# Optimization experiments

Measured on AMD Instinct MI355X. Metric: run time of the kernel, lower is better.

## Reference

```python
import jax, jax.numpy as jnp
import numpy as np

D_MODEL = 1024
N_HEADS = 16
D_HEAD = D_MODEL // N_HEADS
B, T = 2, 2048


def setup_inputs() -> dict:
    key = jax.random.key(0)
    ks = jax.random.split(key, 8)
    s = 1.0 / np.sqrt(D_MODEL)
    return {
        "x": jax.random.normal(ks[0], (B, T, D_MODEL), dtype=jnp.float32),
        "ln_g": jnp.ones((D_MODEL,), jnp.float32),
        "ln_b": jnp.zeros((D_MODEL,), jnp.float32),
        "w_qkv": jax.random.normal(ks[1], (D_MODEL, 3 * D_MODEL), jnp.float32) * s,
        "b_qkv": jnp.zeros((3 * D_MODEL,), jnp.float32),
        "w_gate": jax.random.normal(ks[2], (D_MODEL, D_MODEL), jnp.float32) * s,
        "b_gate": jnp.zeros((D_MODEL,), jnp.float32),
        "w_proj": jax.random.normal(ks[3], (D_MODEL, D_MODEL), jnp.float32) * s,
        "b_proj": jnp.zeros((D_MODEL,), jnp.float32),
    }


def reference(x, ln_g, ln_b, w_qkv, b_qkv, w_gate, b_gate, w_proj, b_proj):
    Bb, Tt, Dd = x.shape
    H, dh = N_HEADS, D_HEAD

    # LayerNorm (eps=1e-5, torch default)
    mu = jnp.mean(x, axis=-1, keepdims=True)
    var = jnp.mean((x - mu) ** 2, axis=-1, keepdims=True)
    x_norm = (x - mu) / jnp.sqrt(var + 1e-5) * ln_g + ln_b

    qkv = x_norm @ w_qkv + b_qkv
    q, k, v = jnp.split(qkv, 3, axis=-1)

    # concept gate on the RAW input x (not x_norm), normalized by its mean
    gate_sig = jax.nn.sigmoid(x @ w_gate + b_gate)
    gate_norm = gate_sig / (jnp.mean(gate_sig, axis=-1, keepdims=True) + 1e-5)
    q = q * gate_norm
    k = k * gate_norm

    # [B,T,D] -> [B,H,T,dh]
    def to_heads(t):
        return t.reshape(Bb, Tt, H, dh).transpose(0, 2, 1, 3)

    q, k, v = to_heads(q), to_heads(k), to_heads(v)

    q = jax.nn.elu(q) + 1.0
    k = jax.nn.elu(k) + 1.0

    # materialized outer-product cumsum (faithful to source formulation)
    kv = jnp.einsum("bhtd,bhtm->bhtdm", k, v)          # [B,H,T,dh,dh]
    kv_cumsum = jnp.cumsum(kv, axis=2)
    out_num = jnp.einsum("bhtd,bhtdm->bhtm", q, kv_cumsum)
    k_cumsum = jnp.cumsum(k, axis=2)
    out_den = jnp.einsum("bhtd,bhtd->bht", q, k_cumsum)[..., None] + 1e-5
    out = out_num / out_den                              # [B,H,T,dh]

    out = out.transpose(0, 2, 1, 3).reshape(Bb, Tt, Dd)
    return out @ w_proj + b_proj
```

## Files before the change

kernel.cpp:

```cpp
#include <hip/hip_runtime.h>
#include <math.h>

constexpr int D      = 1024;
constexpr int H      = 16;
constexpr int DH     = 64;
constexpr int Bb     = 2;
constexpr int T      = 2048;
constexpr int BT     = Bb * T;
constexpr int CHUNK  = 64;
constexpr int NC     = T / CHUNK;
constexpr int LS     = 72;

typedef __attribute__((ext_vector_type(8))) short bf16x8;
typedef __attribute__((ext_vector_type(4))) float f32x4;

#define GLOAD_LDS16(gp, lp) \
    __builtin_amdgcn_global_load_lds((const __attribute__((address_space(1))) void*)(gp), \
                                     (__attribute__((address_space(3))) void*)(lp), 16, 0, 0)

__device__ __forceinline__ short to_bf16(float f) {
    unsigned u = __float_as_uint(f);
    unsigned r = (u + 0x7fffu + ((u >> 16) & 1u)) >> 16;
    return (short)r;
}
__device__ __forceinline__ float bf2f(short s) {
    return __uint_as_float(((unsigned)(unsigned short)s) << 16);
}

__device__ __forceinline__ float block_sum_256(float v, float* sbuf) {
    #pragma unroll
    for (int off = 32; off > 0; off >>= 1) v += __shfl_down(v, off, 64);
    int lane = threadIdx.x & 63;
    int wid  = threadIdx.x >> 6;
    if (lane == 0) sbuf[wid] = v;
    __syncthreads();
    float r = (threadIdx.x < 4) ? sbuf[threadIdx.x] : 0.0f;
    r += __shfl_down(r, 2, 64);
    r += __shfl_down(r, 1, 64);
    if (threadIdx.x == 0) sbuf[0] = r;
    __syncthreads();
    float outv = sbuf[0];
    __syncthreads();
    return outv;
}

__device__ __forceinline__ float elu1(float x) {
    return x > 0.0f ? x + 1.0f : __expf(x);
}

__global__ __launch_bounds__(256) void pre_kernel(const float* __restrict__ x,
                                                  const float* __restrict__ g,
                                                  const float* __restrict__ b,
                                                  const float* __restrict__ wq,
                                                  const float* __restrict__ wg,
                                                  const float* __restrict__ wp,
                                                  short* __restrict__ ynb,
                                                  short* __restrict__ xbb,
                                                  short* __restrict__ wTcomb,
                                                  short* __restrict__ wTp,
                                                  float* __restrict__ gmean) {
    __shared__ float sbuf[4];
    __shared__ short tile[32][33];
    int bid = blockIdx.x;
    if (bid < BT) {
        int row = bid;
        if (threadIdx.x == 0) gmean[row] = 0.0f;
        const float* xr = x + (size_t)row * D;
        int c = threadIdx.x * 4;
        float4 xv = *(const float4*)(xr + c);
        float mu = block_sum_256(xv.x + xv.y + xv.z + xv.w, sbuf) * (1.0f / D);
        float d0 = xv.x - mu, d1 = xv.y - mu, d2 = xv.z - mu, d3 = xv.w - mu;
        float var = block_sum_256(d0*d0 + d1*d1 + d2*d2 + d3*d3, sbuf) * (1.0f / D);
        float rstd = rsqrtf(var + 1e-5f);
        float4 gv = *(const float4*)(g + c);
        float4 bv = *(const float4*)(b + c);
        short4 o, xo;
        o.x = to_bf16(d0 * rstd * gv.x + bv.x);
        o.y = to_bf16(d1 * rstd * gv.y + bv.y);
        o.z = to_bf16(d2 * rstd * gv.z + bv.z);
        o.w = to_bf16(d3 * rstd * gv.w + bv.w);
        xo.x = to_bf16(xv.x); xo.y = to_bf16(xv.y);
        xo.z = to_bf16(xv.z); xo.w = to_bf16(xv.w);
        *(short4*)(ynb + (size_t)row * D + c) = o;
        *(short4*)(xbb + (size_t)row * D + c) = xo;
    } else {
        int t2 = bid - BT;
        const float* W; short* Wt; int N; int t;
        if (t2 < 3072)      { W = wq; Wt = wTcomb;                       N = 3072; t = t2; }
        else if (t2 < 4096) { W = wg; Wt = wTcomb + (size_t)3072 * 1024; N = 1024; t = t2 - 3072; }
        else                { W = wp; Wt = wTp;                          N = 1024; t = t2 - 4096; }
        int ntiles = N >> 5;
        int nb = (t % ntiles) * 32, kb = (t / ntiles) * 32;
        int tx = threadIdx.x & 31, ty = threadIdx.x >> 5;
        #pragma unroll
        for (int i = 0; i < 4; ++i) {
            int k = kb + ty + i * 8;
            tile[ty + i * 8][tx] = to_bf16(W[(size_t)k * N + nb + tx]);
        }
        __syncthreads();
        #pragma unroll
        for (int i = 0; i < 4; ++i) {
            int n = nb + ty + i * 8;
            Wt[(size_t)n * 1024 + kb + tx] = tile[tx][ty + i * 8];
        }
    }
}

__global__ __launch_bounds__(256) void gemm_fused_qkvgate(const short* __restrict__ xnb,
                                                          const short* __restrict__ xb,
                                                          const short* __restrict__ Wt,
                                                          const float* __restrict__ b_qkv,
                                                          const float* __restrict__ b_gate,
                                                          short* __restrict__ qkvb,
                                                          short* __restrict__ sigb,
                                                          float* __restrict__ gmean) {
    constexpr int BK = 32, K = 1024;
    __shared__ short Als[128 * BK];
    __shared__ short Bls[128 * BK];

    const int bid   = blockIdx.x;
    const int xcd   = bid & 7;
    const int local = bid >> 3;
    const int cx = xcd & 3, ry = xcd >> 2;
    const int lx = local & 7, ly = local >> 3;
    const int bxx = cx * 8 + lx;
    const int byy = ry * 16 + ly;

    const int tid  = threadIdx.x;
    const int wave = tid >> 6;
    const int lane = tid & 63;
    const int row0 = byy * 128;
    const int col0 = bxx * 128;
    const bool isg = (col0 >= 3 * D);
    const short* A = isg ? xb : xnb;
    const int wm = (wave & 1) * 64;
    const int wn = (wave >> 1) * 64;

    f32x4 acc[4][4] = {};
    const int srow = lane >> 2;
    const int skk  = (lane & 3) * 8;
    const int fr = lane & 15;
    const int fk = (lane >> 4) * 8;

    for (int k0 = 0; k0 < K; k0 += BK) {
        __syncthreads();
        #pragma unroll
        for (int u = 0; u < 2; ++u) {
            int cchunk = wave * 2 + u;
            int r = cchunk * 16 + srow;
            GLOAD_LDS16(A  + (size_t)(row0 + r) * K + k0 + skk, &Als[cchunk * 512]);
            GLOAD_LDS16(Wt + (size_t)(col0 + r) * K + k0 + skk, &Bls[cchunk * 512]);
        }
        __syncthreads();

        bf16x8 af[4], bfr[4];
        #pragma unroll
        for (int i = 0; i < 4; ++i) {
            af[i]  = *(const bf16x8*)&Als[(wm + i * 16 + fr) * BK + fk];
            bfr[i] = *(const bf16x8*)&Bls[(wn + i * 16 + fr) * BK + fk];
        }
        #pragma unroll
        for (int mi = 0; mi < 4; ++mi)
            #pragma unroll
            for (int ni = 0; ni < 4; ++ni)
                acc[mi][ni] = __builtin_amdgcn_mfma_f32_16x16x32_bf16(af[mi], bfr[ni], acc[mi][ni], 0, 0, 0);
    }

    const int ccol  = lane & 15;
    const int crow4 = (lane >> 4) * 4;
    if (!isg) {
        #pragma unroll
        for (int mi = 0; mi < 4; ++mi) {
            #pragma unroll
            for (int ni = 0; ni < 4; ++ni) {
                int col = col0 + wn + ni * 16 + ccol;
                float bv = b_qkv[col];
                #pragma unroll
                for (int r = 0; r < 4; ++r) {
                    int row = row0 + wm + mi * 16 + crow4 + r;
                    qkvb[(size_t)row * (3 * D) + col] = to_bf16(acc[mi][ni][r] + bv);
                }
            }
        }
    } else {
        #pragma unroll
        for (int mi = 0; mi < 4; ++mi) {
            #pragma unroll
            for (int r = 0; r < 4; ++r) {
                int lrow = wm + mi * 16 + crow4 + r;
                float psum = 0.0f;
                #pragma unroll
                for (int ni = 0; ni < 4; ++ni) {
                    int col = col0 + wn + ni * 16 + ccol - 3 * D;
                    float v = acc[mi][ni][r] + b_gate[col];
                    float sv = 1.0f / (1.0f + __expf(-v));
                    sigb[(size_t)(row0 + lrow) * D + col] = to_bf16(sv);
                    psum += sv;
                }
                psum += __shfl_xor(psum, 1, 64);
                psum += __shfl_xor(psum, 2, 64);
                psum += __shfl_xor(psum, 4, 64);
                psum += __shfl_xor(psum, 8, 64);
                if (ccol == 0) atomicAdd(&gmean[row0 + lrow], psum);
            }
        }
    }
}

__global__ __launch_bounds__(256) void chunk_state_mfma(const short* __restrict__ qkvb,
                                                        const short* __restrict__ sigb,
                                                        const float* __restrict__ gmean,
                                                        float* __restrict__ Sc,
                                                        float* __restrict__ zc) {
    __shared__ short Kt[DH * LS];
    __shared__ short Vt[DH * LS];
    int idx = blockIdx.x;
    int c = idx & (NC - 1), h = (idx >> 5) & (H - 1), b = idx >> 9;
    size_t bt0 = (size_t)b * T + c * CHUNK;
    const short* kbase = qkvb + bt0 * (3 * D) + D + h * DH;
    const short* vbase = kbase + D;
    const short* sbase = sigb + bt0 * D + h * DH;
    int tid = threadIdx.x;

    #pragma unroll
    for (int l = 0; l < 2; ++l) {
        int i  = tid + l * 256;
        int t  = i >> 3;
        int d8 = (i & 7) * 8;
        float invm = 1.0f / (gmean[bt0 + t] * (1.0f / D) + 1e-5f);
        bf16x8 kv = *(const bf16x8*)(kbase + (size_t)t * (3 * D) + d8);
        bf16x8 vv = *(const bf16x8*)(vbase + (size_t)t * (3 * D) + d8);
        bf16x8 sg = *(const bf16x8*)(sbase + (size_t)t * D + d8);
        #pragma unroll
        for (int j = 0; j < 8; ++j) {
            float gn = bf2f(sg[j]) * invm;
            Kt[(d8 + j) * LS + t] = to_bf16(elu1(bf2f(kv[j]) * gn));
            Vt[(d8 + j) * LS + t] = vv[j];
        }
    }
    __syncthreads();

    const int wv = tid >> 6, lane = tid & 63;
    const int fr = lane & 15, quad = lane >> 4;
    const int fk = quad * 8, crow4 = quad * 4, ccol = lane & 15;
    const int mbase = wv * 16;

    bf16x8 af[2];
    af[0] = *(const bf16x8*)&Vt[(mbase + fr) * LS + fk];
    af[1] = *(const bf16x8*)&Vt[(mbase + fr) * LS + 32 + fk];

    f32x4 acc[4] = {};
    #pragma unroll
    for (int n = 0; n < 4; ++n) {
        #pragma unroll
        for (int ck = 0; ck < 2; ++ck) {
            bf16x8 bk = *(const bf16x8*)&Kt[(n * 16 + fr) * LS + ck * 32 + fk];
            acc[n] = __builtin_amdgcn_mfma_f32_16x16x32_bf16(af[ck], bk, acc[n], 0, 0, 0);
        }
    }

    float* Sd = Sc + (size_t)idx * (DH * DH);
    #pragma unroll
    for (int n = 0; n < 4; ++n)
        #pragma unroll
        for (int r = 0; r < 4; ++r)
            Sd[(mbase + crow4 + r) * DH + n * 16 + ccol] = acc[n][r];

    if (tid < DH) {
        float zs = 0.0f;
        for (int t = 0; t < CHUNK; ++t) zs += bf2f(Kt[tid * LS + t]);
        zc[(size_t)idx * DH + tid] = zs;
    }
}

__global__ __launch_bounds__(256) void chunk_prefix_kernel(const float* __restrict__ S,
                                                           short* __restrict__ Spb,
                                                           float* __restrict__ z) {
    int bh   = blockIdx.x >> 4;
    int part = blockIdx.x & 15;
    int e    = part * 256 + threadIdx.x;
    const float* Sb = S + (size_t)bh * NC * DH * DH;
    short* Pb = Spb + (size_t)bh * NC * DH * DH;
    float acc = 0.0f;
    for (int c = 0; c < NC; ++c) {
        size_t off = (size_t)c * DH * DH + e;
        float t = Sb[off];
        Pb[off] = to_bf16(acc);
        acc += t;
    }
    if (part == 0 && threadIdx.x < DH) {
        float* zb = z + (size_t)bh * NC * DH;
        float za = 0.0f;
        for (int c = 0; c < NC; ++c) {
            float* p = zb + c * DH + threadIdx.x;
            float t = *p; *p = za; za += t;
        }
    }
}

__global__ __launch_bounds__(256) void chunk_attn_mfma(const short* __restrict__ qkvb,
                                                       const short* __restrict__ sigb,
                                                       const float* __restrict__ gmean,
                                                       const short* __restrict__ Spb,
                                                       const float* __restrict__ zc,
                                                       short* __restrict__ attnb) {
    __shared__ short Qs[CHUNK * LS];
    __shared__ short Ks[CHUNK * LS];
    __shared__ short Vt[DH * LS];
    __shared__ short Ss[DH * LS];
    __shared__ float zpL[DH];
    __shared__ float den[CHUNK];
    short* As = Ks;

    int idx = blockIdx.x;
    int c = idx & (NC - 1), h = (idx >> 5) & (H - 1), b = idx >> 9;
    size_t bt0 = (size_t)b * T + c * CHUNK;
    const short* qbase = qkvb + bt0 * (3 * D) + h * DH;
    const short* kbase = qbase + D;
    const short* vbase = qbase + 2 * D;
    const short* sbase = sigb + bt0 * D + h * DH;
    const short* spb = Spb + (size_t)idx * (DH * DH);
    int tid = threadIdx.x;

    #pragma unroll
    for (int l = 0; l < 2; ++l) {
        int i  = tid + l * 256;
        int t  = i >> 3;
        int d8 = (i & 7) * 8;
        float invm = 1.0f / (gmean[bt0 + t] * (1.0f / D) + 1e-5f);
        bf16x8 qv = *(const bf16x8*)(qbase + (size_t)t * (3 * D) + d8);
        bf16x8 kv = *(const bf16x8*)(kbase + (size_t)t * (3 * D) + d8);
        bf16x8 vv = *(const bf16x8*)(vbase + (size_t)t * (3 * D) + d8);
        bf16x8 sg = *(const bf16x8*)(sbase + (size_t)t * D + d8);
        bf16x8 qg, kg;
        #pragma unroll
        for (int j = 0; j < 8; ++j) {
            float gn = bf2f(sg[j]) * invm;
            qg[j] = to_bf16(elu1(bf2f(qv[j]) * gn));
            kg[j] = to_bf16(elu1(bf2f(kv[j]) * gn));
            Vt[(d8 + j) * LS + t] = vv[j];
        }
        *(bf16x8*)&Qs[t * LS + d8] = qg;
        *(bf16x8*)&Ks[t * LS + d8] = kg;
        *(bf16x8*)&Ss[t * LS + d8] = *(const bf16x8*)(spb + (size_t)i * 8);
    }
    if (tid < DH) zpL[tid] = zc[(size_t)idx * DH + tid];
    __syncthreads();

    const int wv = tid >> 6, lane = tid & 63;
    const int fr = lane & 15, quad = lane >> 4;
    const int fk = quad * 8, crow4 = quad * 4, ccol = lane & 15;
    const int tbase = wv * 16;

    bf16x8 aq[2];
    aq[0] = *(const bf16x8*)&Qs[(tbase + fr) * LS + fk];
    aq[1] = *(const bf16x8*)&Qs[(tbase + fr) * LS + 32 + fk];

    f32x4 accs[4] = {};
    #pragma unroll
    for (int n = 0; n < 4; ++n) {
        #pragma unroll
        for (int ck = 0; ck < 2; ++ck) {
            bf16x8 bk = *(const bf16x8*)&Ks[(n * 16 + fr) * LS + ck * 32 + fk];
            accs[n] = __builtin_amdgcn_mfma_f32_16x16x32_bf16(aq[ck], bk, accs[n], 0, 0, 0);
        }
    }
    __syncthreads();

    float part[4] = {0.f, 0.f, 0.f, 0.f};
    #pragma unroll
    for (int n = 0; n < 4; ++n) {
        #pragma unroll
        for (int r = 0; r < 4; ++r) {
            int tt = tbase + crow4 + r;
            int ss = n * 16 + ccol;
            float v = (ss <= tt) ? accs[n][r] : 0.0f;
            part[r] += v;
            As[tt * LS + ss] = to_bf16(v);
        }
    }
    #pragma unroll
    for (int r = 0; r < 4; ++r) {
        part[r] += __shfl_xor(part[r], 1, 64);
        part[r] += __shfl_xor(part[r], 2, 64);
        part[r] += __shfl_xor(part[r], 4, 64);
        part[r] += __shfl_xor(part[r], 8, 64);
    }
    if (fr == 0) {
        #pragma unroll
        for (int r = 0; r < 4; ++r) den[tbase + crow4 + r] = part[r];
    }
    __syncthreads();

    if (tid < CHUNK) {
        float qz = 0.0f;
        #pragma unroll 8
        for (int d = 0; d < DH; ++d) qz += bf2f(Qs[tid * LS + d]) * zpL[d];
        den[tid] += qz + 1e-5f;
    }

    f32x4 acco[4] = {};
    #pragma unroll
    for (int m4 = 0; m4 < 4; ++m4) {
        #pragma unroll
        for (int ck = 0; ck < 2; ++ck) {
            bf16x8 bs = *(const bf16x8*)&Ss[(m4 * 16 + fr) * LS + ck * 32 + fk];
            acco[m4] = __builtin_amdgcn_mfma_f32_16x16x32_bf16(aq[ck], bs, acco[m4], 0, 0, 0);
        }
    }
    bf16x8 aa[2];
    aa[0] = *(const bf16x8*)&As[(tbase + fr) * LS + fk];
    aa[1] = *(const bf16x8*)&As[(tbase + fr) * LS + 32 + fk];
    #pragma unroll
    for (int m4 = 0; m4 < 4; ++m4) {
        #pragma unroll
        for (int ck = 0; ck < 2; ++ck) {
            bf16x8 bv = *(const bf16x8*)&Vt[(m4 * 16 + fr) * LS + ck * 32 + fk];
            acco[m4] = __builtin_amdgcn_mfma_f32_16x16x32_bf16(aa[ck], bv, acco[m4], 0, 0, 0);
        }
    }
    __syncthreads();

    short* obase = attnb + bt0 * D + h * DH;
    #pragma unroll
    for (int r = 0; r < 4; ++r) {
        int tt = tbase + crow4 + r;
        float rv = 1.0f / den[tt];
        #pragma unroll
        for (int m4 = 0; m4 < 4; ++m4)
            obase[(size_t)tt * D + m4 * 16 + ccol] = to_bf16(acco[m4][r] * rv);
    }
}

__global__ __launch_bounds__(256) void gemm_proj64(const short* __restrict__ A,
                                                   const short* __restrict__ Bt,
                                                   const float* __restrict__ bias,
                                                   float* __restrict__ C) {
    constexpr int BK = 32, K = 1024, N = 1024;
    __shared__ short Als[64 * BK];
    __shared__ short Bls[128 * BK];

    const int bid   = blockIdx.x;
    const int xcd   = bid & 7;
    const int local = bid >> 3;
    const int cx = xcd & 3, ry = xcd >> 2;
    const int lx = local & 1, ly = local >> 1;
    const int bxx = cx * 2 + lx;
    const int byy = ry * 32 + ly;

    const int tid  = threadIdx.x;
    const int wave = tid >> 6;
    const int lane = tid & 63;
    const int row0 = byy * 64;
    const int col0 = bxx * 128;
    const int wn = wave * 32;

    f32x4 acc[4][2] = {};
    const int srow = lane >> 2;
    const int skk  = (lane & 3) * 8;
    const int fr = lane & 15;
    const int fk = (lane >> 4) * 8;

    for (int k0 = 0; k0 < K; k0 += BK) {
        __syncthreads();
        #pragma unroll
        for (int u = 0; u < 3; ++u) {
            int cc = wave * 3 + u;
            if (cc < 4) {
                int r = cc * 16 + srow;
                GLOAD_LDS16(A + (size_t)(row0 + r) * K + k0 + skk, &Als[cc * 512]);
            } else {
                int c2 = cc - 4;
                int r = c2 * 16 + srow;
                GLOAD_LDS16(Bt + (size_t)(col0 + r) * K + k0 + skk, &Bls[c2 * 512]);
            }
        }
        __syncthreads();

        bf16x8 af[4], bfr[2];
        #pragma unroll
        for (int i = 0; i < 4; ++i)
            af[i] = *(const bf16x8*)&Als[(i * 16 + fr) * BK + fk];
        #pragma unroll
        for (int j = 0; j < 2; ++j)
            bfr[j] = *(const bf16x8*)&Bls[(wn + j * 16 + fr) * BK + fk];
        #pragma unroll
        for (int mi = 0; mi < 4; ++mi)
            #pragma unroll
            for (int ni = 0; ni < 2; ++ni)
                acc[mi][ni] = __builtin_amdgcn_mfma_f32_16x16x32_bf16(af[mi], bfr[ni], acc[mi][ni], 0, 0, 0);
    }

    const int ccol  = lane & 15;
    const int crow4 = (lane >> 4) * 4;
    #pragma unroll
    for (int mi = 0; mi < 4; ++mi) {
        #pragma unroll
        for (int ni = 0; ni < 2; ++ni) {
            int col = col0 + wn + ni * 16 + ccol;
            float bv = bias[col];
            #pragma unroll
            for (int r = 0; r < 4; ++r) {
                int row = row0 + mi * 16 + crow4 + r;
                C[(size_t)row * N + col] = acc[mi][ni][r] + bv;
            }
        }
    }
}

extern "C" void kernel_launch(void* const* d_in, const int* in_sizes, int n_in,
                              void* d_out, int out_size, void* d_ws, size_t ws_size,
                              hipStream_t stream) {
    const float* x      = (const float*)d_in[0];
    const float* ln_g   = (const float*)d_in[1];
    const float* ln_b   = (const float*)d_in[2];
    const float* w_qkv  = (const float*)d_in[3];
    const float* b_qkv  = (const float*)d_in[4];
    const float* w_gate = (const float*)d_in[5];
    const float* b_gate = (const float*)d_in[6];
    const float* w_proj = (const float*)d_in[7];
    const float* b_proj = (const float*)d_in[8];
    float* out = (float*)d_out;

    short* xnb   = (short*)d_ws;
    short* xb    = xnb + (size_t)BT * D;
    short* wTc   = xb + (size_t)BT * D;
    short* wTp   = wTc + (size_t)4096 * 1024;
    short* qkvb  = wTp + (size_t)D * D;
    short* sigb  = qkvb + (size_t)BT * 3 * D;
    short* attnb = sigb + (size_t)BT * D;
    float* zc    = (float*)(attnb + (size_t)BT * D);
    float* gmean = zc + (size_t)Bb * H * NC * DH;
    float* Sc    = (float*)xnb;
    short* Spb   = wTc;

    pre_kernel<<<BT + 5120, 256, 0, stream>>>(x, ln_g, ln_b, w_qkv, w_gate, w_proj,
                                              xnb, xb, wTc, wTp, gmean);
    gemm_fused_qkvgate<<<1024, 256, 0, stream>>>(
        xnb, xb, wTc, b_qkv, b_gate, qkvb, sigb, gmean);
    chunk_state_mfma<<<Bb * H * NC, 256, 0, stream>>>(qkvb, sigb, gmean, Sc, zc);
    chunk_prefix_kernel<<<Bb * H * 16, 256, 0, stream>>>(Sc, Spb, zc);
    chunk_attn_mfma<<<Bb * H * NC, 256, 0, stream>>>(qkvb, sigb, gmean, Spb, zc, attnb);
    gemm_proj64<<<512, 256, 0, stream>>>(attnb, wTp, b_proj, out);
}
```

Measured before the change: 207.2 us.

## Rewrite fused QKV/gate GEMM with 256x256 tiles and double-buffered swizzled LDS pipeline

Replaces the 128x128, BK=32 fused QKV+gate GEMM with a 256x256-tile, 512-thread kernel that stages 64-wide K slices into double-buffered LDS using direct global-to-LDS loads. It adds an XOR swizzle on the LDS layout to avoid bank conflicts, interleaves the prefetch of later tiles with MFMA groups using explicit vmcnt waits and barriers, and raises MFMA priority with s_setprio. The aim is to hide memory latency and increase operand reuse per block. The cost is only 256 blocks, which gives lower occupancy and a fragile hand-tuned wait schedule that depends on exact load counts.

```diff
diff --git a/kernel.cpp b/kernel.cpp
--- a/kernel.cpp
+++ b/kernel.cpp
@@ -106,102 +106,158 @@
     }
 }
 
-__global__ __launch_bounds__(256) void gemm_fused_qkvgate(const short* __restrict__ xnb,
-                                                          const short* __restrict__ xb,
-                                                          const short* __restrict__ Wt,
-                                                          const float* __restrict__ b_qkv,
-                                                          const float* __restrict__ b_gate,
-                                                          short* __restrict__ qkvb,
-                                                          short* __restrict__ sigb,
-                                                          float* __restrict__ gmean) {
-    constexpr int BK = 32, K = 1024;
-    __shared__ short Als[128 * BK];
-    __shared__ short Bls[128 * BK];
+#define SWZ(os) ((os) ^ ((((os) >> 6) & 3) << 3))
+#define BARX() __builtin_amdgcn_s_barrier()
+#define LGKM0() asm volatile("s_waitcnt lgkmcnt(0)" ::: "memory")
+#define VMW(n) asm volatile("s_waitcnt vmcnt(" #n ")" ::: "memory")
+#define MEMFENCE() asm volatile("" ::: "memory")
+
+#define STG(Mp, rb, t, kc, isB) do {                                                       \
+    short* _b = ldsbuf + ((((t) & 1)) << 15) + (((((isB) << 1) | (kc))) << 13) + wid * 1024; \
+    const short* _g = (Mp) + (size_t)((rb) + wid * 32 + s_r) * 1024 + (t) * 64 + (kc) * 32 + s_c; \
+    GLOAD_LDS16(_g, _b);                                                                   \
+    GLOAD_LDS16(_g + (size_t)16 * 1024, _b + 512);                                         \
+} while (0)
+
+#define FRAGA(t, kc, mi) (*(const bf16x8*)(ldsbuf + (((t) & 1) << 15) + ((kc) << 13) + \
+    SWZ((wm * 128 + (mi) * 16 + fr) * 32 + fk)))
+#define FRAGB(t, kc, ni) (*(const bf16x8*)(ldsbuf + (((t) & 1) << 15) + ((2 + (kc)) << 13) + \
+    SWZ((wn * 64 + (ni) * 16 + fr) * 32 + fk)))
+
+#define GROUP(t, S1, S2, S3, S4, W2, W4) do {                                              \
+    bf16x8 af[8], bq[4];                                                                   \
+                                                                    \
+    _Pragma("unroll") for (int mi = 0; mi < 8; ++mi) af[mi] = FRAGA(t, 0, mi);             \
+    bq[0] = FRAGB(t, 0, 0); bq[1] = FRAGB(t, 0, 1);                                        \
+    if (S1) STG(Wt, col0, (t) + 1, 1, 1);                                                  \
+    BARX(); LGKM0();                                                                       \
+    __builtin_amdgcn_s_setprio(1);                                                         \
+    _Pragma("unroll") for (int mi = 0; mi < 8; ++mi) {                                     \
+        acc[mi][0] = __builtin_amdgcn_mfma_f32_16x16x32_bf16(af[mi], bq[0], acc[mi][0], 0, 0, 0); \
+        acc[mi][1] = __builtin_amdgcn_mfma_f32_16x16x32_bf16(af[mi], bq[1], acc[mi][1], 0, 0, 0); \
+    }                                                                                      \
+    __builtin_amdgcn_s_setprio(0);                                                         \
+    BARX();                                                                                \
+                                                                    \
+    bq[2] = FRAGB(t, 0, 2); bq[3] = FRAGB(t, 0, 3);                                        \
+    if (S2) STG(Ap, row0, (t) + 2, 0, 0);                                                  \
+    BARX(); LGKM0();                                                                       \
+    __builtin_amdgcn_s_setprio(1);                                                         \
+    _Pragma("unroll") for (int mi = 0; mi < 8; ++mi) {                                     \
+        acc[mi][2] = __builtin_amdgcn_mfma_f32_16x16x32_bf16(af[mi], bq[2], acc[mi][2], 0, 0, 0); \
+        acc[mi][3] = __builtin_amdgcn_mfma_f32_16x16x32_bf16(af[mi], bq[3], acc[mi][3], 0, 0, 0); \
+    }                                                                                      \
+    __builtin_amdgcn_s_setprio(0);                                                         \
+    W2; BARX();                                                                            \
+                                                                    \
+    _Pragma("unroll") for (int mi = 0; mi < 8; ++mi) af[mi] = FRAGA(t, 1, mi);             \
+    bq[0] = FRAGB(t, 1, 0); bq[1] = FRAGB(t, 1, 1);                                        \
+    if (S3) STG(Wt, col0, (t) + 2, 0, 1);                                                  \
+    BARX(); LGKM0();                                                                       \
+    __builtin_amdgcn_s_setprio(1);                                                         \
+    _Pragma("unroll") for (int mi = 0; mi < 8; ++mi) {                                     \
+        acc[mi][0] = __builtin_amdgcn_mfma_f32_16x16x32_bf16(af[mi], bq[0], acc[mi][0], 0, 0, 0); \
+        acc[mi][1] = __builtin_amdgcn_mfma_f32_16x16x32_bf16(af[mi], bq[1], acc[mi][1], 0, 0, 0); \
+    }                                                                                      \
+    __builtin_amdgcn_s_setprio(0);                                                         \
+    BARX();                                                                                \
+                                                                    \
+    bq[2] = FRAGB(t, 1, 2); bq[3] = FRAGB(t, 1, 3);                                        \
+    if (S4) STG(Ap, row0, (t) + 2, 1, 0);                                                  \
+    BARX(); LGKM0();                                                                       \
+    __builtin_amdgcn_s_setprio(1);                                                         \
+    _Pragma("unroll") for (int mi = 0; mi < 8; ++mi) {                                     \
+        acc[mi][2] = __builtin_amdgcn_mfma_f32_16x16x32_bf16(af[mi], bq[2], acc[mi][2], 0, 0, 0); \
+        acc[mi][3] = __builtin_amdgcn_mfma_f32_16x16x32_bf16(af[mi], bq[3], acc[mi][3], 0, 0, 0); \
+    }                                                                                      \
+    __builtin_amdgcn_s_setprio(0);                                                         \
+    W4; BARX();                                                                            \
+} while (0)
+
+__global__ __launch_bounds__(512, 2) void gemm_fused_qkvgate(const short* __restrict__ xnb,
+                                                             const short* __restrict__ xb,
+                                                             const short* __restrict__ Wt,
+                                                             const float* __restrict__ b_qkv,
+                                                             const float* __restrict__ b_gate,
+                                                             short* __restrict__ qkvb,
+                                                             short* __restrict__ sigb,
+                                                             float* __restrict__ gmean) {
+    __shared__ short ldsbuf[2 * 32768];
 
     const int bid   = blockIdx.x;
     const int xcd   = bid & 7;
     const int local = bid >> 3;
     const int cx = xcd & 3, ry = xcd >> 2;
-    const int lx = local & 7, ly = local >> 3;
-    const int bxx = cx * 8 + lx;
-    const int byy = ry * 16 + ly;
+    const int bxx = cx * 4 + (local & 3);
+    const int byy = ry * 8 + (local >> 2);
+    const int row0 = byy * 256;
+    const int col0 = bxx * 256;
+    const bool isg = (col0 >= 3 * D);
+    const short* Ap = isg ? xb : xnb;
 
     const int tid  = threadIdx.x;
-    const int wave = tid >> 6;
+    const int wid  = tid >> 6;
     const int lane = tid & 63;
-    const int row0 = byy * 128;
-    const int col0 = bxx * 128;
-    const bool isg = (col0 >= 3 * D);
-    const short* A = isg ? xb : xnb;
-    const int wm = (wave & 1) * 64;
-    const int wn = (wave >> 1) * 64;
-
-    f32x4 acc[4][4] = {};
-    const int srow = lane >> 2;
-    const int skk  = (lane & 3) * 8;
+    const int wm = wid >> 2;
+    const int wn = wid & 3;
     const int fr = lane & 15;
     const int fk = (lane >> 4) * 8;
 
-    for (int k0 = 0; k0 < K; k0 += BK) {
-        __syncthreads();
-        #pragma unroll
-        for (int u = 0; u < 2; ++u) {
-            int cchunk = wave * 2 + u;
-            int r = cchunk * 16 + srow;
-            GLOAD_LDS16(A  + (size_t)(row0 + r) * K + k0 + skk, &Als[cchunk * 512]);
-            GLOAD_LDS16(Wt + (size_t)(col0 + r) * K + k0 + skk, &Bls[cchunk * 512]);
-        }
-        __syncthreads();
-
-        bf16x8 af[4], bfr[4];
-        #pragma unroll
-        for (int i = 0; i < 4; ++i) {
-            af[i]  = *(const bf16x8*)&Als[(wm + i * 16 + fr) * BK + fk];
-            bfr[i] = *(const bf16x8*)&Bls[(wn + i * 16 + fr) * BK + fk];
-        }
-        #pragma unroll
-        for (int mi = 0; mi < 4; ++mi)
-            #pragma unroll
-            for (int ni = 0; ni < 4; ++ni)
-                acc[mi][ni] = __builtin_amdgcn_mfma_f32_16x16x32_bf16(af[mi], bfr[ni], acc[mi][ni], 0, 0, 0);
-    }
+    const int s_r = lane >> 2;
+    const int s_c = 8 * ((lane & 3) ^ ((lane >> 3) & 3));
+
+    f32x4 acc[8][4] = {};
+
+    STG(Ap, row0, 0, 0, 0); MEMFENCE();
+    STG(Wt, col0, 0, 0, 1); MEMFENCE();
+    STG(Ap, row0, 0, 1, 0); MEMFENCE();
+    STG(Wt, col0, 0, 1, 1); MEMFENCE();
+    STG(Ap, row0, 1, 0, 0); MEMFENCE();
+    STG(Wt, col0, 1, 0, 1); MEMFENCE();
+    STG(Ap, row0, 1, 1, 0);
+    VMW(10);
+    BARX();
+
+    for (int t = 0; t < 14; ++t) GROUP(t, 1, 1, 1, 1, VMW(10), VMW(10));
+    GROUP(14, 1, 0, 0, 0, VMW(8), VMW(4));
+    GROUP(15, 0, 0, 0, 0, VMW(0), (void)0);
 
     const int ccol  = lane & 15;
     const int crow4 = (lane >> 4) * 4;
     if (!isg) {
         #pragma unroll
-        for (int mi = 0; mi < 4; ++mi) {
+        for (int mi = 0; mi < 8; ++mi) {
             #pragma unroll
             for (int ni = 0; ni < 4; ++ni) {
-                int col = col0 + wn + ni * 16 + ccol;
+                int col = col0 + wn * 64 + ni * 16 + ccol;
                 float bv = b_qkv[col];
                 #pragma unroll
                 for (int r = 0; r < 4; ++r) {
-                    int row = row0 + wm + mi * 16 + crow4 + r;
+                    int row = row0 + wm * 128 + mi * 16 + crow4 + r;
                     qkvb[(size_t)row * (3 * D) + col] = to_bf16(acc[mi][ni][r] + bv);
                 }
             }
         }
     } else {
         #pragma unroll
-        for (int mi = 0; mi < 4; ++mi) {
+        for (int mi = 0; mi < 8; ++mi) {
             #pragma unroll
             for (int r = 0; r < 4; ++r) {
-                int lrow = wm + mi * 16 + crow4 + r;
+                int lrow = row0 + wm * 128 + mi * 16 + crow4 + r;
                 float psum = 0.0f;
                 #pragma unroll
                 for (int ni = 0; ni < 4; ++ni) {
-                    int col = col0 + wn + ni * 16 + ccol - 3 * D;
+                    int col = col0 + wn * 64 + ni * 16 + ccol - 3 * D;
                     float v = acc[mi][ni][r] + b_gate[col];
                     float sv = 1.0f / (1.0f + __expf(-v));
-                    sigb[(size_t)(row0 + lrow) * D + col] = to_bf16(sv);
+                    sigb[(size_t)lrow * D + col] = to_bf16(sv);
                     psum += sv;
                 }
                 psum += __shfl_xor(psum, 1, 64);
                 psum += __shfl_xor(psum, 2, 64);
                 psum += __shfl_xor(psum, 4, 64);
                 psum += __shfl_xor(psum, 8, 64);
-                if (ccol == 0) atomicAdd(&gmean[row0 + lrow], psum);
+                if (ccol == 0) atomicAdd(&gmean[lrow], psum);
             }
         }
     }
@@ -536,7 +592,7 @@
 
     pre_kernel<<<BT + 5120, 256, 0, stream>>>(x, ln_g, ln_b, w_qkv, w_gate, w_proj,
                                               xnb, xb, wTc, wTp, gmean);
-    gemm_fused_qkvgate<<<1024, 256, 0, stream>>>(
+    gemm_fused_qkvgate<<<256, 512, 0, stream>>>(
         xnb, xb, wTc, b_qkv, b_gate, qkvb, sigb, gmean);
     chunk_state_mfma<<<Bb * H * NC, 256, 0, stream>>>(qkvb, sigb, gmean, Sc, zc);
     chunk_prefix_kernel<<<Bb * H * 16, 256, 0, stream>>>(Sc, Spb, zc);
```

Result: faster. 191.2 us (-7.7%).
